# Kernel optimization log

Measured on AMD Instinct MI355X. Metric: run time of the kernel, lower is better.

Reference implementation:

```python
import jax, jax.numpy as jnp
import numpy as np

DIM_LATENT = 256
NUM_ATOM_TYPES = 16
NUM_EDGE_TYPES = 4
HIDDEN = 256
HIDDEN_FINAL = 256
BS, N = 8, 256


def setup_inputs() -> dict:
    key = jax.random.key(0)
    ks = jax.random.split(key, 12)
    s = lambda fan_in: 1.0 / np.sqrt(fan_in)
    return {
        "latent": jax.random.normal(ks[0], (BS, N, DIM_LATENT), jnp.float32),
        "positions": jax.random.normal(ks[1], (BS, N, 3), jnp.float32),
        "atom_types": jax.random.uniform(ks[2], (BS, N, NUM_ATOM_TYPES), jnp.float32),
        # latent_mlp: Linear(dim_latent, hidden) -> ReLU -> Linear(hidden, hidden)
        "W1": jax.random.uniform(ks[3], (DIM_LATENT, HIDDEN), jnp.float32, -s(DIM_LATENT), s(DIM_LATENT)),
        "b1": jax.random.uniform(ks[4], (HIDDEN,), jnp.float32, -s(DIM_LATENT), s(DIM_LATENT)),
        "W2": jax.random.uniform(ks[5], (HIDDEN, HIDDEN), jnp.float32, -s(HIDDEN), s(HIDDEN)),
        "b2": jax.random.uniform(ks[6], (HIDDEN,), jnp.float32, -s(HIDDEN), s(HIDDEN)),
        # final_mlp: Linear(1+num_atom_types+dim_latent, hidden_final) -> ReLU -> Linear(hidden_final, num_edge_types)
        "W3": jax.random.uniform(ks[7], (1 + NUM_ATOM_TYPES + DIM_LATENT, HIDDEN_FINAL), jnp.float32, -s(1 + NUM_ATOM_TYPES + DIM_LATENT), s(1 + NUM_ATOM_TYPES + DIM_LATENT)),
        "b3": jax.random.uniform(ks[8], (HIDDEN_FINAL,), jnp.float32, -s(1 + NUM_ATOM_TYPES + DIM_LATENT), s(1 + NUM_ATOM_TYPES + DIM_LATENT)),
        "W4": jax.random.uniform(ks[9], (HIDDEN_FINAL, NUM_EDGE_TYPES), jnp.float32, -s(HIDDEN_FINAL), s(HIDDEN_FINAL)),
        "b4": jax.random.uniform(ks[10], (NUM_EDGE_TYPES,), jnp.float32, -s(HIDDEN_FINAL), s(HIDDEN_FINAL)),
    }


def _pairwise_dist(positions):
    # torch.cdist (euclidean), grad-safe sqrt (zero on the diagonal)
    diff = positions[:, :, None, :] - positions[:, None, :, :]  # bs x n x n x 3
    d2 = jnp.sum(diff * diff, axis=-1)
    safe = jnp.where(d2 > 0, d2, 1.0)
    return jnp.where(d2 > 0, jnp.sqrt(safe), 0.0)


def reference(latent, positions, atom_types, W1, b1, W2, b2, W3, b3, W4, b4):
    # latent_mlp
    h = jax.nn.relu(latent @ W1 + b1) @ W2 + b2  # bs x n x hidden (== dim_latent)
    dist = _pairwise_dist(positions)[..., None]  # bs x n x n x 1
    atom_pairs = atom_types[:, :, None, :] * atom_types[:, None, :, :]  # bs x n x n x A
    latent_pairs = h[:, :, None, :] * h[:, None, :, :]                  # bs x n x n x C
    y = jnp.concatenate((dist, atom_pairs, latent_pairs), axis=3)
    return jax.nn.relu(y @ W3 + b3) @ W4 + b4  # bs x n x n x num_edge_types
```

## Files before the change

kernel.cpp:

```cpp
#include <hip/hip_runtime.h>

#define DIM 256
#define NA 16
#define NE 4
#define KTOT 288

typedef __attribute__((ext_vector_type(8))) short short8;
typedef __attribute__((ext_vector_type(4))) float f32x4;

static __device__ __forceinline__ ushort f2bf(float f) {
  union { float f; unsigned int u; } v; v.f = f;
  unsigned int r = (v.u + 0x7FFFu + ((v.u >> 16) & 1u)) >> 16;
  return (ushort)r;
}

static __device__ __forceinline__ float bf2f(ushort s) {
  union { unsigned int u; float f; } v; v.u = ((unsigned int)s) << 16;
  return v.f;
}

static __device__ __forceinline__ unsigned cvtpk(float lo, float hi) {
  unsigned r;
  asm("v_cvt_pk_bf16_f32 %0, %1, %2" : "=v"(r) : "v"(lo), "v"(hi));
  return r;
}

static __device__ __forceinline__ void gll16(const void* g, void* l) {
  __builtin_amdgcn_global_load_lds((const __attribute__((address_space(1))) void*)g,
                                   (__attribute__((address_space(3))) void*)l, 16, 0, 0);
}

__global__ __launch_bounds__(256) void prep_h_kernel(
    const float* __restrict__ latent, const float* __restrict__ atoms,
    const float* __restrict__ W1, const float* __restrict__ b1,
    const float* __restrict__ W2, const float* __restrict__ b2,
    float* __restrict__ h_out, ushort* __restrict__ G_out) {
  __shared__ float lat[8][DIM];
  __shared__ float t1[8][DIM];
  const int b = blockIdx.x >> 5, i0 = (blockIdx.x & 31) * 8;
  const int k = threadIdx.x;
  #pragma unroll
  for (int r = 0; r < 8; ++r) lat[r][k] = latent[(b*256 + i0 + r) * DIM + k];
  __syncthreads();
  float acc[8];
  #pragma unroll
  for (int r = 0; r < 8; ++r) acc[r] = b1[k];
  for (int c = 0; c < DIM; c += 4) {
    float w0 = W1[(c+0)*DIM + k], w1 = W1[(c+1)*DIM + k];
    float w2 = W1[(c+2)*DIM + k], w3 = W1[(c+3)*DIM + k];
    #pragma unroll
    for (int r = 0; r < 8; ++r) {
      const float4 l4 = *reinterpret_cast<const float4*>(&lat[r][c]);
      acc[r] += l4.x*w0 + l4.y*w1 + l4.z*w2 + l4.w*w3;
    }
  }
  #pragma unroll
  for (int r = 0; r < 8; ++r) t1[r][k] = fmaxf(acc[r], 0.f);
  __syncthreads();
  #pragma unroll
  for (int r = 0; r < 8; ++r) acc[r] = b2[k];
  for (int c = 0; c < DIM; c += 4) {
    float w0 = W2[(c+0)*DIM + k], w1 = W2[(c+1)*DIM + k];
    float w2 = W2[(c+2)*DIM + k], w3 = W2[(c+3)*DIM + k];
    #pragma unroll
    for (int r = 0; r < 8; ++r) {
      const float4 l4 = *reinterpret_cast<const float4*>(&t1[r][c]);
      acc[r] += l4.x*w0 + l4.y*w1 + l4.z*w2 + l4.w*w3;
    }
  }
  #pragma unroll
  for (int r = 0; r < 8; ++r) {
    int row = b*256 + i0 + r;
    h_out[row*DIM + k] = acc[r];
    G_out[row*KTOT + NA + k] = f2bf(acc[r]);
  }
  if (k < NA) {
    #pragma unroll
    for (int r = 0; r < 8; ++r) {
      int row = b*256 + i0 + r;
      G_out[row*KTOT + k] = f2bf(atoms[row*NA + k]);
      G_out[row*KTOT + 272 + k] = 0;
    }
  }
}

__global__ __launch_bounds__(256) void prep_w3t_kernel(
    const float* __restrict__ W3, ushort* __restrict__ W3T) {
  const int kk = blockIdx.x, c = threadIdx.x;
  W3T[kk*KTOT + c] = (c < 272) ? f2bf(W3[(1+c)*DIM + kk]) : (ushort)0;
  if (c < 32) {
    int c2 = 256 + c;
    W3T[kk*KTOT + c2] = (c2 < 272) ? f2bf(W3[(1+c2)*DIM + kk]) : (ushort)0;
  }
}

__global__ __attribute__((amdgpu_flat_work_group_size(512,512), amdgpu_waves_per_eu(2,2)))
void edge_main_kernel(
    const float* __restrict__ positions,
    const float* __restrict__ W3, const float* __restrict__ b3,
    const float* __restrict__ W4, const float* __restrict__ b4,
    const ushort* __restrict__ G, const ushort* __restrict__ W3T,
    float* __restrict__ out) {
  __shared__ union UU {
    char w3t[2][16384];
    float partial[4][256][4];
  } u;
  __shared__ char y_lds[2][16384];
  __shared__ float dist_lds[256];

  const int bid = blockIdx.x;
  const int b = bid / 136;
  int q = bid - b*136;
  int it = 0;
  while (q >= 16 - it) { q -= 16 - it; ++it; }
  const int jt = it + q;
  const int i0 = b*256 + it*16, j0 = b*256 + jt*16;

  const int tid = threadIdx.x;
  const int lane = tid & 63, w = tid >> 6;
  const int wn = w & 3;
  const int wp = w >> 2;
  const int c15 = lane & 15, hi = lane >> 4;

  if (tid < 256) {
    int pi = tid >> 4, pj = tid & 15;
    const float* pa = &positions[(i0 + pi)*3];
    const float* pb = &positions[(j0 + pj)*3];
    float dx = pa[0]-pb[0], dy = pa[1]-pb[1], dz = pa[2]-pb[2];
    float d2 = dx*dx + dy*dy + dz*dz;
    dist_lds[tid] = d2 > 0.f ? sqrtf(d2) : 0.f;
  }

  auto stage = [&](int kk) {
    #pragma unroll
    for (int qq = 0; qq < 2; ++qq) {
      int s0 = w*8 + qq*4;
      int sub = s0 + hi;
      int nt_ = sub >> 2, oct = sub & 3;
      const ushort* src = &W3T[(size_t)(nt_*16 + c15)*KTOT + kk*32 + oct*8];
      gll16(src, u.w3t[kk & 1] + s0*256);
    }
  };

  const int pair_ = tid >> 1, po = tid & 1;
  const int pi_ = pair_ >> 4, pj_ = pair_ & 15;
  const ushort* giBase = &G[(size_t)(i0 + pi_)*KTOT + po*16];
  const ushort* gjBase = &G[(size_t)(j0 + pj_)*KTOT + po*16];

  short8 yi0, yi1, yj0, yj1;
  auto y_load = [&](int kk) {
    yi0 = *reinterpret_cast<const short8*>(giBase + kk*32);
    yi1 = *reinterpret_cast<const short8*>(giBase + kk*32 + 8);
    yj0 = *reinterpret_cast<const short8*>(gjBase + kk*32);
    yj1 = *reinterpret_cast<const short8*>(gjBase + kk*32 + 8);
  };
  auto y_finish = [&](int kk) {
    union { ushort us[8]; short8 s8; } A0, A1, B0, B1;
    A0.s8 = yi0; A1.s8 = yi1; B0.s8 = yj0; B1.s8 = yj1;
    uint4 p0, p1;
    p0.x = cvtpk(bf2f(A0.us[0])*bf2f(B0.us[0]), bf2f(A0.us[1])*bf2f(B0.us[1]));
    p0.y = cvtpk(bf2f(A0.us[2])*bf2f(B0.us[2]), bf2f(A0.us[3])*bf2f(B0.us[3]));
    p0.z = cvtpk(bf2f(A0.us[4])*bf2f(B0.us[4]), bf2f(A0.us[5])*bf2f(B0.us[5]));
    p0.w = cvtpk(bf2f(A0.us[6])*bf2f(B0.us[6]), bf2f(A0.us[7])*bf2f(B0.us[7]));
    p1.x = cvtpk(bf2f(A1.us[0])*bf2f(B1.us[0]), bf2f(A1.us[1])*bf2f(B1.us[1]));
    p1.y = cvtpk(bf2f(A1.us[2])*bf2f(B1.us[2]), bf2f(A1.us[3])*bf2f(B1.us[3]));
    p1.z = cvtpk(bf2f(A1.us[4])*bf2f(B1.us[4]), bf2f(A1.us[5])*bf2f(B1.us[5]));
    p1.w = cvtpk(bf2f(A1.us[6])*bf2f(B1.us[6]), bf2f(A1.us[7])*bf2f(B1.us[7]));
    char* dst = y_lds[kk & 1] + pi_*1024 + po*512 + pj_*16;
    *reinterpret_cast<uint4*>(dst) = p0;
    *reinterpret_cast<uint4*>(dst + 256) = p1;
  };

  f32x4 acc[4][8];
  #pragma unroll
  for (int at = 0; at < 4; ++at)
    #pragma unroll
    for (int bt = 0; bt < 8; ++bt) { acc[at][bt].x=0.f; acc[at][bt].y=0.f; acc[at][bt].z=0.f; acc[at][bt].w=0.f; }

  stage(0);
  y_load(0);
  y_finish(0);
  __syncthreads();

  #pragma unroll
  for (int kk = 0; kk < 9; ++kk) {
    if (kk < 8) { y_load(kk + 1); stage(kk + 1); }
    {
      const char* ap = u.w3t[kk & 1];
      const char* bp = y_lds[kk & 1];
      short8 afr[4];
      #pragma unroll
      for (int at = 0; at < 4; ++at)
        afr[at] = *reinterpret_cast<const short8*>(ap + (wn*4 + at)*1024 + lane*16);
      #pragma unroll
      for (int bt = 0; bt < 8; ++bt) {
        short8 bb = *reinterpret_cast<const short8*>(bp + (wp*8 + bt)*1024 + lane*16);
        acc[0][bt] = __builtin_amdgcn_mfma_f32_16x16x32_bf16(afr[0], bb, acc[0][bt], 0, 0, 0);
        acc[1][bt] = __builtin_amdgcn_mfma_f32_16x16x32_bf16(afr[1], bb, acc[1][bt], 0, 0, 0);
        acc[2][bt] = __builtin_amdgcn_mfma_f32_16x16x32_bf16(afr[2], bb, acc[2][bt], 0, 0, 0);
        acc[3][bt] = __builtin_amdgcn_mfma_f32_16x16x32_bf16(afr[3], bb, acc[3][bt], 0, 0, 0);
      }
    }
    if (kk < 8) y_finish(kk + 1);
    __syncthreads();
  }

  __builtin_amdgcn_sched_barrier(0);

  float b3v[4][4], w30v[4][4]; float4 w4v[4][4];
  #pragma unroll
  for (int at = 0; at < 4; ++at)
    #pragma unroll
    for (int r = 0; r < 4; ++r) {
      int n = (wn*4 + at)*16 + hi*4 + r;
      b3v[at][r]  = b3[n];
      w30v[at][r] = W3[n];
      w4v[at][r]  = *reinterpret_cast<const float4*>(&W4[n*4]);
    }
  #pragma unroll
  for (int bt = 0; bt < 8; ++bt) {
    int pair = wp*128 + bt*16 + c15;
    float d = dist_lds[pair];
    float4 pe; pe.x=0.f; pe.y=0.f; pe.z=0.f; pe.w=0.f;
    #pragma unroll
    for (int at = 0; at < 4; ++at)
      #pragma unroll
      for (int r = 0; r < 4; ++r) {
        float z  = acc[at][bt][r] + d*w30v[at][r] + b3v[at][r];
        float rz = fmaxf(z, 0.f);
        pe.x += rz*w4v[at][r].x; pe.y += rz*w4v[at][r].y;
        pe.z += rz*w4v[at][r].z; pe.w += rz*w4v[at][r].w;
      }
    pe.x += __shfl_xor(pe.x, 16); pe.y += __shfl_xor(pe.y, 16);
    pe.z += __shfl_xor(pe.z, 16); pe.w += __shfl_xor(pe.w, 16);
    pe.x += __shfl_xor(pe.x, 32); pe.y += __shfl_xor(pe.y, 32);
    pe.z += __shfl_xor(pe.z, 32); pe.w += __shfl_xor(pe.w, 32);
    if (hi == 0) *reinterpret_cast<float4*>(&u.partial[wn][pair][0]) = pe;
  }
  __syncthreads();
  if (tid < 256) {
    int pair = tid;
    float4 v;
    v.x = u.partial[0][pair][0] + u.partial[1][pair][0] + u.partial[2][pair][0] + u.partial[3][pair][0];
    v.y = u.partial[0][pair][1] + u.partial[1][pair][1] + u.partial[2][pair][1] + u.partial[3][pair][1];
    v.z = u.partial[0][pair][2] + u.partial[1][pair][2] + u.partial[2][pair][2] + u.partial[3][pair][2];
    v.w = u.partial[0][pair][3] + u.partial[1][pair][3] + u.partial[2][pair][3] + u.partial[3][pair][3];
    const float4 bv = *reinterpret_cast<const float4*>(b4);
    v.x += bv.x; v.y += bv.y; v.z += bv.z; v.w += bv.w;
    int il = it*16 + (pair >> 4);
    int jl = jt*16 + (pair & 15);
    *reinterpret_cast<float4*>(&out[(((size_t)b*256 + il)*256 + jl)*NE]) = v;
    if (it != jt)
      *reinterpret_cast<float4*>(&out[(((size_t)b*256 + jl)*256 + il)*NE]) = v;
  }
}

extern "C" void kernel_launch(void* const* d_in, const int* in_sizes, int n_in,
                              void* d_out, int out_size, void* d_ws, size_t ws_size,
                              hipStream_t stream) {
  const float* latent    = (const float*)d_in[0];
  const float* positions = (const float*)d_in[1];
  const float* atoms     = (const float*)d_in[2];
  const float* W1 = (const float*)d_in[3];
  const float* b1 = (const float*)d_in[4];
  const float* W2 = (const float*)d_in[5];
  const float* b2 = (const float*)d_in[6];
  const float* W3 = (const float*)d_in[7];
  const float* b3 = (const float*)d_in[8];
  const float* W4 = (const float*)d_in[9];
  const float* b4 = (const float*)d_in[10];
  float* out = (float*)d_out;

  char* ws = (char*)d_ws;
  float*  h_ws   = (float*)ws;
  ushort* G_ws   = (ushort*)(ws + 2097152);
  ushort* W3T_ws = (ushort*)(ws + 2097152 + 1179648);

  hipLaunchKernelGGL(prep_h_kernel, dim3(256), dim3(256), 0, stream,
                     latent, atoms, W1, b1, W2, b2, h_ws, G_ws);
  hipLaunchKernelGGL(prep_w3t_kernel, dim3(256), dim3(256), 0, stream, W3, W3T_ws);
  hipLaunchKernelGGL(edge_main_kernel, dim3(1088), dim3(512), 0, stream,
                     positions, W3, b3, W4, b4, G_ws, W3T_ws, out);
}
```

Baseline: 109.8 us.

## Split edge tiles into four 64-pair blocks to raise occupancy

Each block of the edge kernel now handles a 4x16 slice of pairs instead of a 16x16 tile, so the grid grows fourfold and per-thread accumulators drop from 32 to 8 MFMA tiles. The launch bounds now ask for 4 waves per EU and LDS for the y tiles shrinks, aiming at more concurrent blocks to hide latency. In exchange, every block restages the full W3T operand, so W3 traffic and A-fragment LDS reads per pair rise about fourfold and the MFMA-to-load ratio falls.

```diff
diff --git a/kernel.cpp b/kernel.cpp
--- a/kernel.cpp
+++ b/kernel.cpp
@@ -6,7 +6,9 @@
 #define KTOT 288
 
 typedef __attribute__((ext_vector_type(8))) short short8;
+typedef __attribute__((ext_vector_type(4))) short short4v;
 typedef __attribute__((ext_vector_type(4))) float f32x4;
+typedef __attribute__((ext_vector_type(2))) unsigned int uint2v;
 
 static __device__ __forceinline__ ushort f2bf(float f) {
   union { float f; unsigned int u; } v; v.f = f;
@@ -94,7 +96,7 @@
   }
 }
 
-__global__ __attribute__((amdgpu_flat_work_group_size(512,512), amdgpu_waves_per_eu(2,2)))
+__global__ __attribute__((amdgpu_flat_work_group_size(512,512), amdgpu_waves_per_eu(4,4)))
 void edge_main_kernel(
     const float* __restrict__ positions,
     const float* __restrict__ W3, const float* __restrict__ b3,
@@ -103,18 +105,21 @@
     float* __restrict__ out) {
   __shared__ union UU {
     char w3t[2][16384];
-    float partial[4][256][4];
+    float partial[4][64][4];
   } u;
-  __shared__ char y_lds[2][16384];
-  __shared__ float dist_lds[256];
+  __shared__ char y_lds[2][4096];
+  __shared__ float dist_lds[64];
 
   const int bid = blockIdx.x;
-  const int b = bid / 136;
-  int q = bid - b*136;
+  const int b = bid / 544;
+  int rem = bid - b*544;
+  const int wg4 = rem & 3;
+  int q = rem >> 2;
   int it = 0;
   while (q >= 16 - it) { q -= 16 - it; ++it; }
   const int jt = it + q;
   const int i0 = b*256 + it*16, j0 = b*256 + jt*16;
+  const int pbase = wg4*4;
 
   const int tid = threadIdx.x;
   const int lane = tid & 63, w = tid >> 6;
@@ -122,9 +127,9 @@
   const int wp = w >> 2;
   const int c15 = lane & 15, hi = lane >> 4;
 
-  if (tid < 256) {
+  if (tid < 64) {
     int pi = tid >> 4, pj = tid & 15;
-    const float* pa = &positions[(i0 + pi)*3];
+    const float* pa = &positions[(i0 + pbase + pi)*3];
     const float* pb = &positions[(j0 + pj)*3];
     float dx = pa[0]-pb[0], dy = pa[1]-pb[1], dz = pa[2]-pb[2];
     float d2 = dx*dx + dy*dy + dz*dz;
@@ -142,40 +147,31 @@
     }
   };
 
-  const int pair_ = tid >> 1, po = tid & 1;
-  const int pi_ = pair_ >> 4, pj_ = pair_ & 15;
-  const ushort* giBase = &G[(size_t)(i0 + pi_)*KTOT + po*16];
-  const ushort* gjBase = &G[(size_t)(j0 + pj_)*KTOT + po*16];
-
-  short8 yi0, yi1, yj0, yj1;
+  const int pr = tid >> 3, s = tid & 7;
+  const int pi_ = pr >> 4, pj_ = pr & 15;
+  const ushort* giRow = &G[(size_t)(i0 + pbase + pi_)*KTOT + s*4];
+  const ushort* gjRow = &G[(size_t)(j0 + pj_)*KTOT + s*4];
+
+  short4v yi, yj;
   auto y_load = [&](int kk) {
-    yi0 = *reinterpret_cast<const short8*>(giBase + kk*32);
-    yi1 = *reinterpret_cast<const short8*>(giBase + kk*32 + 8);
-    yj0 = *reinterpret_cast<const short8*>(gjBase + kk*32);
-    yj1 = *reinterpret_cast<const short8*>(gjBase + kk*32 + 8);
+    yi = *reinterpret_cast<const short4v*>(giRow + kk*32);
+    yj = *reinterpret_cast<const short4v*>(gjRow + kk*32);
   };
   auto y_finish = [&](int kk) {
-    union { ushort us[8]; short8 s8; } A0, A1, B0, B1;
-    A0.s8 = yi0; A1.s8 = yi1; B0.s8 = yj0; B1.s8 = yj1;
-    uint4 p0, p1;
-    p0.x = cvtpk(bf2f(A0.us[0])*bf2f(B0.us[0]), bf2f(A0.us[1])*bf2f(B0.us[1]));
-    p0.y = cvtpk(bf2f(A0.us[2])*bf2f(B0.us[2]), bf2f(A0.us[3])*bf2f(B0.us[3]));
-    p0.z = cvtpk(bf2f(A0.us[4])*bf2f(B0.us[4]), bf2f(A0.us[5])*bf2f(B0.us[5]));
-    p0.w = cvtpk(bf2f(A0.us[6])*bf2f(B0.us[6]), bf2f(A0.us[7])*bf2f(B0.us[7]));
-    p1.x = cvtpk(bf2f(A1.us[0])*bf2f(B1.us[0]), bf2f(A1.us[1])*bf2f(B1.us[1]));
-    p1.y = cvtpk(bf2f(A1.us[2])*bf2f(B1.us[2]), bf2f(A1.us[3])*bf2f(B1.us[3]));
-    p1.z = cvtpk(bf2f(A1.us[4])*bf2f(B1.us[4]), bf2f(A1.us[5])*bf2f(B1.us[5]));
-    p1.w = cvtpk(bf2f(A1.us[6])*bf2f(B1.us[6]), bf2f(A1.us[7])*bf2f(B1.us[7]));
-    char* dst = y_lds[kk & 1] + pi_*1024 + po*512 + pj_*16;
-    *reinterpret_cast<uint4*>(dst) = p0;
-    *reinterpret_cast<uint4*>(dst + 256) = p1;
+    union { ushort us[4]; short4v s4; } A, B;
+    A.s4 = yi; B.s4 = yj;
+    uint2v p;
+    p.x = cvtpk(bf2f(A.us[0])*bf2f(B.us[0]), bf2f(A.us[1])*bf2f(B.us[1]));
+    p.y = cvtpk(bf2f(A.us[2])*bf2f(B.us[2]), bf2f(A.us[3])*bf2f(B.us[3]));
+    char* dst = y_lds[kk & 1] + pi_*1024 + (s >> 1)*256 + pj_*16 + (s & 1)*8;
+    *reinterpret_cast<uint2v*>(dst) = p;
   };
 
-  f32x4 acc[4][8];
+  f32x4 acc[4][2];
   #pragma unroll
   for (int at = 0; at < 4; ++at)
     #pragma unroll
-    for (int bt = 0; bt < 8; ++bt) { acc[at][bt].x=0.f; acc[at][bt].y=0.f; acc[at][bt].z=0.f; acc[at][bt].w=0.f; }
+    for (int bt = 0; bt < 2; ++bt) { acc[at][bt].x=0.f; acc[at][bt].y=0.f; acc[at][bt].z=0.f; acc[at][bt].w=0.f; }
 
   stage(0);
   y_load(0);
@@ -193,8 +189,8 @@
       for (int at = 0; at < 4; ++at)
         afr[at] = *reinterpret_cast<const short8*>(ap + (wn*4 + at)*1024 + lane*16);
       #pragma unroll
-      for (int bt = 0; bt < 8; ++bt) {
-        short8 bb = *reinterpret_cast<const short8*>(bp + (wp*8 + bt)*1024 + lane*16);
+      for (int bt = 0; bt < 2; ++bt) {
+        short8 bb = *reinterpret_cast<const short8*>(bp + (wp*2 + bt)*1024 + lane*16);
         acc[0][bt] = __builtin_amdgcn_mfma_f32_16x16x32_bf16(afr[0], bb, acc[0][bt], 0, 0, 0);
         acc[1][bt] = __builtin_amdgcn_mfma_f32_16x16x32_bf16(afr[1], bb, acc[1][bt], 0, 0, 0);
         acc[2][bt] = __builtin_amdgcn_mfma_f32_16x16x32_bf16(afr[2], bb, acc[2][bt], 0, 0, 0);
@@ -218,8 +214,8 @@
       w4v[at][r]  = *reinterpret_cast<const float4*>(&W4[n*4]);
     }
   #pragma unroll
-  for (int bt = 0; bt < 8; ++bt) {
-    int pair = wp*128 + bt*16 + c15;
+  for (int bt = 0; bt < 2; ++bt) {
+    int pair = (wp*2 + bt)*16 + c15;
     float d = dist_lds[pair];
     float4 pe; pe.x=0.f; pe.y=0.f; pe.z=0.f; pe.w=0.f;
     #pragma unroll
@@ -238,7 +234,7 @@
     if (hi == 0) *reinterpret_cast<float4*>(&u.partial[wn][pair][0]) = pe;
   }
   __syncthreads();
-  if (tid < 256) {
+  if (tid < 64) {
     int pair = tid;
     float4 v;
     v.x = u.partial[0][pair][0] + u.partial[1][pair][0] + u.partial[2][pair][0] + u.partial[3][pair][0];
@@ -247,7 +243,7 @@
     v.w = u.partial[0][pair][3] + u.partial[1][pair][3] + u.partial[2][pair][3] + u.partial[3][pair][3];
     const float4 bv = *reinterpret_cast<const float4*>(b4);
     v.x += bv.x; v.y += bv.y; v.z += bv.z; v.w += bv.w;
-    int il = it*16 + (pair >> 4);
+    int il = it*16 + pbase + (pair >> 4);
     int jl = jt*16 + (pair & 15);
     *reinterpret_cast<float4*>(&out[(((size_t)b*256 + il)*256 + jl)*NE]) = v;
     if (it != jt)
@@ -279,6 +275,6 @@
   hipLaunchKernelGGL(prep_h_kernel, dim3(256), dim3(256), 0, stream,
                      latent, atoms, W1, b1, W2, b2, h_ws, G_ws);
   hipLaunchKernelGGL(prep_w3t_kernel, dim3(256), dim3(256), 0, stream, W3, W3T_ws);
-  hipLaunchKernelGGL(edge_main_kernel, dim3(1088), dim3(512), 0, stream,
+  hipLaunchKernelGGL(edge_main_kernel, dim3(4352), dim3(512), 0, stream,
                      positions, W3, b3, W4, b4, G_ws, W3T_ws, out);
 }
```

Result: slower. 191.1 us (+74.0%).
